# Kernel tuning notes

Hardware: AMD Instinct MI355X
Metric: run time of the kernel (lower is better)

Reference implementation:

```python
import jax, jax.numpy as jnp
import numpy as np

M, K = 3072, 768          # hardcoded in the torch module's forward
B, S = 8, 2048            # batch, sequence length
NNZ_PER_ROW = 230
NNZ = M * NNZ_PER_ROW


def setup_inputs() -> dict:
    key = jax.random.key(0)
    k1, k2, k3 = jax.random.split(key, 3)
    rng = np.random.default_rng(0)
    # unique, sorted column indices per row (valid CSR with fixed row nnz)
    cols = np.argsort(rng.random((M, K)), axis=1)[:, :NNZ_PER_ROW]
    cols = np.sort(cols, axis=1).astype(np.int32)
    column_indices = jnp.asarray(cols.reshape(-1))
    row_offsets = jnp.asarray((np.arange(M + 1) * NNZ_PER_ROW).astype(np.int32))
    # diffsort(row_offsets): rows sorted by nnz descending (all equal -> identity)
    row_indices = jnp.arange(M, dtype=jnp.int32)
    values = jax.random.normal(k1, (NNZ,), dtype=jnp.float32) * 0.02
    bias = jax.random.normal(k2, (M,), dtype=jnp.float32) * 0.02
    x = jax.random.normal(k3, (B, S, K), dtype=jnp.float32)
    return {"values": values, "bias": bias, "x": x,
            "row_indices": row_indices, "row_offsets": row_offsets,
            "column_indices": column_indices}


def reference(values, bias, x, row_indices, row_offsets, column_indices):
    # CSR [M, K] sparse weight times dense x: out = x @ W^T + bias
    # (left_spmm(m,k,...,x^T) gives [B, M, S]; .transpose(1,2) -> [B, S, M])
    nnz = values.shape[0]
    # row id of each nonzero from the CSR offsets
    row_ids = jnp.searchsorted(row_offsets, jnp.arange(nnz, dtype=row_offsets.dtype), side="right") - 1
    # scatter values into the (small) dense [M, K] weight; .add sums duplicates
    # exactly as SpMM accumulation would
    W = jnp.zeros((M, K), dtype=values.dtype).at[row_ids, column_indices].add(values)
    out = jnp.einsum("bsk,mk->bsm", x, W) + bias  # [B, S, M]
    return out
```

## Files before the change

kernel.cpp:

```cpp
#include <hip/hip_runtime.h>
#include <hip/hip_bf16.h>
#include <cstdint>

#define K_DIM 768
#define M_DIM 3072
#define BS_TOTAL 16384
#define BK 32
#define KT 24

typedef __attribute__((ext_vector_type(4))) float f32x4;
typedef __attribute__((ext_vector_type(8))) short bf16x8;
typedef __attribute__((ext_vector_type(4))) unsigned short u16x4;
typedef __attribute__((ext_vector_type(4))) float fv4;

typedef unsigned int u32_g __attribute__((address_space(1)));
typedef unsigned int u32_l __attribute__((address_space(3)));

static __device__ __forceinline__ void async_load16(const void* g, void* l) {
    __builtin_amdgcn_global_load_lds((const u32_g*)g, (u32_l*)l, 16, 0, 0);
}

#define BAR() __builtin_amdgcn_s_barrier()
#define SCHEDB() __builtin_amdgcn_sched_barrier(0)

static __device__ __forceinline__ unsigned short f2bf(float f) {
    unsigned u = __builtin_bit_cast(unsigned, f);
    u += 0x7fffu + ((u >> 16) & 1u);
    return (unsigned short)(u >> 16);
}

__global__ void densify_kernel(const float* __restrict__ values,
                               const int* __restrict__ row_offsets,
                               const int* __restrict__ column_indices,
                               unsigned short* __restrict__ Wb) {
    const int r = blockIdx.x;
    const int t = threadIdx.x;
    unsigned int* wrow32 = (unsigned int*)(Wb + (size_t)r * K_DIM);
    for (int i = t; i < K_DIM / 2; i += 256) wrow32[i] = 0u;
    __syncthreads();
    const int start = row_offsets[r], end = row_offsets[r + 1];
    unsigned short* wrow = Wb + (size_t)r * K_DIM;
    for (int i = start + t; i < end; i += 256)
        wrow[column_indices[i]] = f2bf(values[i]);
}

__global__ void convert_x_kernel(const float* __restrict__ x,
                                 unsigned short* __restrict__ xb, int n4) {
    int i = blockIdx.x * 256 + threadIdx.x;
    if (i < n4) {
        fv4 v = ((const fv4*)x)[i];
        u16x4 o;
        o[0] = f2bf(v[0]); o[1] = f2bf(v[1]); o[2] = f2bf(v[2]); o[3] = f2bf(v[3]);
        ((u16x4*)xb)[i] = o;
    }
}


#define STAGE_A(buf, t)                                                         \
    { _Pragma("unroll") for (int c = 0; c < 2; ++c) {                           \
        const int u = c * 256 + tid;                                            \
        const int row = u >> 2;                                                 \
        const int gs = (u & 3) ^ ((row >> 1) & 3);                              \
        async_load16(X + (size_t)(row0 + row) * K_DIM + (t) * BK + gs * 8,      \
                     &sm[buf][0][(size_t)u * 8]); } }

#define STAGE_B(buf, t)                                                         \
    { _Pragma("unroll") for (int c = 0; c < 2; ++c) {                           \
        const int u = c * 256 + tid;                                            \
        const int row = u >> 2;                                                 \
        const int gs = (u & 3) ^ ((row >> 1) & 3);                              \
        async_load16(W + (size_t)(col0 + row) * K_DIM + (t) * BK + gs * 8,      \
                     &sm[buf][1][(size_t)u * 8]); } }

#define LDA(buf)                                                                \
    { _Pragma("unroll") for (int mi = 0; mi < 4; ++mi) {                        \
        const int row = wm * 64 + mi * 16 + fr;                                 \
        const int blk = kq ^ ((row >> 1) & 3);                                  \
        aq[mi] = *(const bf16x8*)&sm[buf][0][row * BK + blk * 8]; } }

#define LDB(buf)                                                                \
    { _Pragma("unroll") for (int ni = 0; ni < 4; ++ni) {                        \
        const int row = wn * 64 + ni * 16 + fr;                                 \
        const int blk = kq ^ ((row >> 1) & 3);                                  \
        bq[ni] = *(const bf16x8*)&sm[buf][1][row * BK + blk * 8]; } }

#define MFMA16()                                                                \
    { __builtin_amdgcn_s_setprio(1);                                            \
      _Pragma("unroll") for (int mi = 0; mi < 4; ++mi)                          \
      _Pragma("unroll") for (int ni = 0; ni < 4; ++ni)                          \
        acc[mi][ni] = __builtin_amdgcn_mfma_f32_16x16x32_bf16(                  \
            aq[mi], bq[ni], acc[mi][ni], 0, 0, 0);                              \
      __builtin_amdgcn_s_setprio(0); }

__global__ __launch_bounds__(256, 4) void gemm_kernel(
    const unsigned short* __restrict__ X,
    const unsigned short* __restrict__ W,
    const float* __restrict__ bias,
    float* __restrict__ out) {
    __shared__ __align__(16) unsigned short sm[2][2][128 * BK];

    const int nwg = gridDim.x;
    int bid = blockIdx.x;
    bid = (bid & 7) * (nwg >> 3) + (bid >> 3);
    const int bx = bid % (M_DIM / 128);
    const int by = bid / (M_DIM / 128);
    const int row0 = by * 128;
    const int col0 = bx * 128;

    const int tid  = threadIdx.x;
    const int lane = tid & 63;
    const int wave = tid >> 6;
    const int wm = wave >> 1;
    const int wn = wave & 1;
    const int fr = lane & 15;
    const int kq = lane >> 4;

    f32x4 acc[4][4] = {};
    bf16x8 aq[4], bq[4];

    STAGE_A(0, 0);
    STAGE_B(0, 0);
    asm volatile("s_waitcnt vmcnt(0)" ::: "memory");
    SCHEDB();
    BAR();

    for (int t = 0; t < KT; ++t) {
        const int buf = t & 1, nbuf = buf ^ 1;
        LDA(buf);
        LDB(buf);
        if (t + 1 < KT) { STAGE_A(nbuf, t + 1); STAGE_B(nbuf, t + 1); }
        BAR();
        MFMA16();
        asm volatile("s_waitcnt vmcnt(0)" ::: "memory");
        SCHEDB();
        BAR();
    }

    float bv[4];
#pragma unroll
    for (int ni = 0; ni < 4; ++ni) bv[ni] = bias[col0 + wn * 64 + ni * 16 + fr];

    const int orow0 = row0 + wm * 64 + kq * 4;
#pragma unroll
    for (int mi = 0; mi < 4; ++mi)
#pragma unroll
        for (int j = 0; j < 4; ++j) {
            float* op = out + (size_t)(orow0 + mi * 16 + j) * M_DIM + col0 + wn * 64 + fr;
#pragma unroll
            for (int ni = 0; ni < 4; ++ni)
                __builtin_nontemporal_store(acc[mi][ni][j] + bv[ni], op + ni * 16);
        }
}

extern "C" void kernel_launch(void* const* d_in, const int* in_sizes, int n_in,
                              void* d_out, int out_size, void* d_ws, size_t ws_size,
                              hipStream_t stream) {
    const float* values         = (const float*)d_in[0];
    const float* bias           = (const float*)d_in[1];
    const float* x              = (const float*)d_in[2];
    const int*   row_offsets    = (const int*)d_in[4];
    const int*   column_indices = (const int*)d_in[5];

    unsigned short* Wb = (unsigned short*)d_ws;
    unsigned short* Xb = (unsigned short*)((char*)d_ws + (size_t)M_DIM * K_DIM * 2);

    densify_kernel<<<M_DIM, 256, 0, stream>>>(values, row_offsets, column_indices, Wb);

    const int n4 = BS_TOTAL * K_DIM / 4;
    convert_x_kernel<<<(n4 + 255) / 256, 256, 0, stream>>>(x, Xb, n4);

    const int grid = (BS_TOTAL / 128) * (M_DIM / 128);
    gemm_kernel<<<grid, 256, 0, stream>>>(Xb, Wb, bias, (float*)d_out);
}
```

Before: 124.2 us.

## Enlarge GEMM tile to 128x256, triple-buffer LDS, fuse prep kernels

Fuses weight densification and x-to-bf16 conversion into one launch. Widens the GEMM block tile from 128x128 to 128x256, with each wave computing a 128x64 slice so every wave reads the whole A tile. The K loop moves from double to triple buffering: it prefetches two stages ahead and waits with vmcnt(6) instead of draining all loads each iteration, and one barrier per step replaces two. The goal is less global traffic per FLOP, better latency hiding and fewer launches, at the cost of more registers and LDS (occupancy bound lowered to 2) and a reordered block-to-tile mapping.

```diff
diff --git a/kernel.cpp b/kernel.cpp
--- a/kernel.cpp
+++ b/kernel.cpp
@@ -5,6 +5,8 @@
 #define K_DIM 768
 #define M_DIM 3072
 #define BS_TOTAL 16384
+#define BM 128
+#define BN 256
 #define BK 32
 #define KT 24
 
@@ -29,29 +31,31 @@
     return (unsigned short)(u >> 16);
 }
 
-__global__ void densify_kernel(const float* __restrict__ values,
-                               const int* __restrict__ row_offsets,
-                               const int* __restrict__ column_indices,
-                               unsigned short* __restrict__ Wb) {
-    const int r = blockIdx.x;
+__global__ void prep_kernel(const float* __restrict__ values,
+                            const int* __restrict__ row_offsets,
+                            const int* __restrict__ column_indices,
+                            unsigned short* __restrict__ Wb,
+                            const float* __restrict__ x,
+                            unsigned short* __restrict__ xb, int n4) {
+    const int b = blockIdx.x;
     const int t = threadIdx.x;
-    unsigned int* wrow32 = (unsigned int*)(Wb + (size_t)r * K_DIM);
-    for (int i = t; i < K_DIM / 2; i += 256) wrow32[i] = 0u;
-    __syncthreads();
-    const int start = row_offsets[r], end = row_offsets[r + 1];
-    unsigned short* wrow = Wb + (size_t)r * K_DIM;
-    for (int i = start + t; i < end; i += 256)
-        wrow[column_indices[i]] = f2bf(values[i]);
-}
-
-__global__ void convert_x_kernel(const float* __restrict__ x,
-                                 unsigned short* __restrict__ xb, int n4) {
-    int i = blockIdx.x * 256 + threadIdx.x;
-    if (i < n4) {
-        fv4 v = ((const fv4*)x)[i];
-        u16x4 o;
-        o[0] = f2bf(v[0]); o[1] = f2bf(v[1]); o[2] = f2bf(v[2]); o[3] = f2bf(v[3]);
-        ((u16x4*)xb)[i] = o;
+    if (b < M_DIM) {
+        const int r = b;
+        unsigned int* wrow32 = (unsigned int*)(Wb + (size_t)r * K_DIM);
+        for (int i = t; i < K_DIM / 2; i += 256) wrow32[i] = 0u;
+        __syncthreads();
+        const int start = row_offsets[r], end = row_offsets[r + 1];
+        unsigned short* wrow = Wb + (size_t)r * K_DIM;
+        for (int i = start + t; i < end; i += 256)
+            wrow[column_indices[i]] = f2bf(values[i]);
+    } else {
+        const int i = (b - M_DIM) * 256 + t;
+        if (i < n4) {
+            fv4 v = ((const fv4*)x)[i];
+            u16x4 o;
+            o[0] = f2bf(v[0]); o[1] = f2bf(v[1]); o[2] = f2bf(v[2]); o[3] = f2bf(v[3]);
+            ((u16x4*)xb)[i] = o;
+        }
     }
 }
 
@@ -62,87 +66,88 @@
         const int row = u >> 2;                                                 \
         const int gs = (u & 3) ^ ((row >> 1) & 3);                              \
         async_load16(X + (size_t)(row0 + row) * K_DIM + (t) * BK + gs * 8,      \
-                     &sm[buf][0][(size_t)u * 8]); } }
+                     &sa[buf][(size_t)u * 8]); } }
 
 #define STAGE_B(buf, t)                                                         \
-    { _Pragma("unroll") for (int c = 0; c < 2; ++c) {                           \
+    { _Pragma("unroll") for (int c = 0; c < 4; ++c) {                           \
         const int u = c * 256 + tid;                                            \
         const int row = u >> 2;                                                 \
         const int gs = (u & 3) ^ ((row >> 1) & 3);                              \
         async_load16(W + (size_t)(col0 + row) * K_DIM + (t) * BK + gs * 8,      \
-                     &sm[buf][1][(size_t)u * 8]); } }
+                     &sb[buf][(size_t)u * 8]); } }
 
 #define LDA(buf)                                                                \
-    { _Pragma("unroll") for (int mi = 0; mi < 4; ++mi) {                        \
-        const int row = wm * 64 + mi * 16 + fr;                                 \
+    { _Pragma("unroll") for (int mi = 0; mi < 8; ++mi) {                        \
+        const int row = mi * 16 + fr;                                           \
         const int blk = kq ^ ((row >> 1) & 3);                                  \
-        aq[mi] = *(const bf16x8*)&sm[buf][0][row * BK + blk * 8]; } }
+        aq[mi] = *(const bf16x8*)&sa[buf][row * BK + blk * 8]; } }
 
 #define LDB(buf)                                                                \
     { _Pragma("unroll") for (int ni = 0; ni < 4; ++ni) {                        \
         const int row = wn * 64 + ni * 16 + fr;                                 \
         const int blk = kq ^ ((row >> 1) & 3);                                  \
-        bq[ni] = *(const bf16x8*)&sm[buf][1][row * BK + blk * 8]; } }
+        bq[ni] = *(const bf16x8*)&sb[buf][row * BK + blk * 8]; } }
 
-#define MFMA16()                                                                \
+#define MFMA32()                                                                \
     { __builtin_amdgcn_s_setprio(1);                                            \
-      _Pragma("unroll") for (int mi = 0; mi < 4; ++mi)                          \
+      _Pragma("unroll") for (int mi = 0; mi < 8; ++mi)                          \
       _Pragma("unroll") for (int ni = 0; ni < 4; ++ni)                          \
         acc[mi][ni] = __builtin_amdgcn_mfma_f32_16x16x32_bf16(                  \
             aq[mi], bq[ni], acc[mi][ni], 0, 0, 0);                              \
       __builtin_amdgcn_s_setprio(0); }
 
-__global__ __launch_bounds__(256, 4) void gemm_kernel(
+__global__ __launch_bounds__(256, 2) void gemm_kernel(
     const unsigned short* __restrict__ X,
     const unsigned short* __restrict__ W,
     const float* __restrict__ bias,
     float* __restrict__ out) {
-    __shared__ __align__(16) unsigned short sm[2][2][128 * BK];
+    __shared__ __align__(16) unsigned short sa[3][BM * BK];
+    __shared__ __align__(16) unsigned short sb[3][BN * BK];
 
     const int nwg = gridDim.x;
     int bid = blockIdx.x;
     bid = (bid & 7) * (nwg >> 3) + (bid >> 3);
-    const int bx = bid % (M_DIM / 128);
-    const int by = bid / (M_DIM / 128);
-    const int row0 = by * 128;
-    const int col0 = bx * 128;
+    const int by = bid % (BS_TOTAL / BM);
+    const int bx = bid / (BS_TOTAL / BM);
+    const int row0 = by * BM;
+    const int col0 = bx * BN;
 
     const int tid  = threadIdx.x;
     const int lane = tid & 63;
-    const int wave = tid >> 6;
-    const int wm = wave >> 1;
-    const int wn = wave & 1;
-    const int fr = lane & 15;
-    const int kq = lane >> 4;
+    const int wn   = tid >> 6;
+    const int fr   = lane & 15;
+    const int kq   = lane >> 4;
 
-    f32x4 acc[4][4] = {};
-    bf16x8 aq[4], bq[4];
-
-    STAGE_A(0, 0);
-    STAGE_B(0, 0);
-    asm volatile("s_waitcnt vmcnt(0)" ::: "memory");
-    SCHEDB();
-    BAR();
-
-    for (int t = 0; t < KT; ++t) {
-        const int buf = t & 1, nbuf = buf ^ 1;
-        LDA(buf);
-        LDB(buf);
-        if (t + 1 < KT) { STAGE_A(nbuf, t + 1); STAGE_B(nbuf, t + 1); }
-        BAR();
-        MFMA16();
-        asm volatile("s_waitcnt vmcnt(0)" ::: "memory");
-        SCHEDB();
-        BAR();
-    }
+    f32x4 acc[8][4] = {};
+    bf16x8 aq[8], bq[4];
 
     float bv[4];
 #pragma unroll
     for (int ni = 0; ni < 4; ++ni) bv[ni] = bias[col0 + wn * 64 + ni * 16 + fr];
 
-    const int orow0 = row0 + wm * 64 + kq * 4;
+    STAGE_A(0, 0); STAGE_B(0, 0);
+    STAGE_A(1, 1); STAGE_B(1, 1);
+    asm volatile("s_waitcnt vmcnt(6)" ::: "memory");
+    SCHEDB();
+    BAR();
+
+    for (int t = 0; t < KT; ++t) {
+        const int buf = t % 3;
+        if (t + 2 < KT) {
+            const int pbuf = (t + 2) % 3;
+            STAGE_A(pbuf, t + 2); STAGE_B(pbuf, t + 2);
+        }
+        LDA(buf);
+        LDB(buf);
+        MFMA32();
+        if (t + 2 < KT)      { asm volatile("s_waitcnt vmcnt(6)" ::: "memory"); SCHEDB(); }
+        else if (t + 1 < KT) { asm volatile("s_waitcnt vmcnt(0)" ::: "memory"); SCHEDB(); }
+        BAR();
+    }
+
+    const int orow0 = row0 + kq * 4;
 #pragma unroll
-    for (int mi = 0; mi < 4; ++mi)
+    for (int mi = 0; mi < 8; ++mi)
 #pragma unroll
         for (int j = 0; j < 4; ++j) {
             float* op = out + (size_t)(orow0 + mi * 16 + j) * M_DIM + col0 + wn * 64 + fr;
@@ -164,11 +169,11 @@
     unsigned short* Wb = (unsigned short*)d_ws;
     unsigned short* Xb = (unsigned short*)((char*)d_ws + (size_t)M_DIM * K_DIM * 2);
 
-    densify_kernel<<<M_DIM, 256, 0, stream>>>(values, row_offsets, column_indices, Wb);
+    const int n4 = BS_TOTAL * K_DIM / 4;
+    const int prep_blocks = M_DIM + (n4 + 255) / 256;
+    prep_kernel<<<prep_blocks, 256, 0, stream>>>(values, row_offsets, column_indices,
+                                                 Wb, x, Xb, n4);
 
-    const int n4 = BS_TOTAL * K_DIM / 4;
-    convert_x_kernel<<<(n4 + 255) / 256, 256, 0, stream>>>(x, Xb, n4);
-
-    const int grid = (BS_TOTAL / 128) * (M_DIM / 128);
+    const int grid = (BS_TOTAL / BM) * (M_DIM / BN);
     gemm_kernel<<<grid, 256, 0, stream>>>(Xb, Wb, bias, (float*)d_out);
 }
```

Measured after the change: 133.7 us. +7.7%, slower.
